# Kernel optimization log

Hardware: AMD Instinct MI355X
Metric: run time of the kernel (lower is better)

## Reference

```python
import jax, jax.numpy as jnp
import numpy as np

B, H, Q, K, D = 2, 8, 512, 512, 64


def setup_inputs() -> dict:
    key = jax.random.key(0)
    ks = jax.random.split(key, 8)
    s = 1.0 / np.sqrt(D)
    return {
        "query": jax.random.normal(ks[0], (B, H, Q, D), dtype=jnp.float32),
        "keys": jax.random.normal(ks[1], (B, H, K, D), dtype=jnp.float32),
        "Wa_w": jax.random.normal(ks[2], (D, D), dtype=jnp.float32) * s,
        "Wa_b": jax.random.normal(ks[3], (D,), dtype=jnp.float32) * s,
        "Ua_w": jax.random.normal(ks[4], (D, D), dtype=jnp.float32) * s,
        "Ua_b": jax.random.normal(ks[5], (D,), dtype=jnp.float32) * s,
        "V_w": jax.random.normal(ks[6], (D,), dtype=jnp.float32) * s,
        "V_b": jax.random.normal(ks[7], (1,), dtype=jnp.float32) * s,
    }


def reference(query, keys, Wa_w, Wa_b, Ua_w, Ua_b, V_w, V_b):
    # Linear projections (torch Linear: x @ W.T + b)
    q_proj = jnp.einsum("bhqd,ed->bhqe", query, Wa_w) + Wa_b  # [B,H,Q,D]
    k_proj = jnp.einsum("bhkd,ed->bhke", keys, Ua_w) + Ua_b   # [B,H,K,D]
    # Broadcast add + tanh -> [B,H,Q,K,D] (the fusion-headroom intermediate)
    features = jnp.tanh(q_proj[:, :, :, None, :] + k_proj[:, :, None, :, :])
    # Linear reduce D -> scalar, squeeze last dim
    scores = jnp.einsum("bhqkd,d->bhqk", features, V_w) + V_b[0]  # [B,H,Q,K]
    return scores
```

## Files before the change

kernel.cpp:

```cpp
#include <hip/hip_runtime.h>


#define BHX 16
#define SEQ 512
#define DDIM 64
#define QT 32
#define KT 64

typedef float f4 __attribute__((ext_vector_type(4)));

__global__ __launch_bounds__(256) void proj_kernel(
    const float* __restrict__ query, const float* __restrict__ keys,
    const float* __restrict__ Wa_w,  const float* __restrict__ Wa_b,
    const float* __restrict__ Ua_w,  const float* __restrict__ Ua_b,
    float* __restrict__ eq, float* __restrict__ gk)
{
  const int t = threadIdx.x, lane = t & 63, wave = t >> 6;
  const bool is_k = blockIdx.x >= 512;
  const float* __restrict__ X  = is_k ? keys : query;
  const float* __restrict__ W  = is_k ? Ua_w : Wa_w;
  const float* __restrict__ Bv = is_k ? Ua_b : Wa_b;
  float* __restrict__ out      = is_k ? gk : eq;
  const int row0 = (blockIdx.x & 511) * 16;

  float w[64];
  const float4* W4 = (const float4*)(W + lane * DDIM);
#pragma unroll
  for (int i = 0; i < 16; ++i) {
    float4 v = W4[i];
    w[4*i] = v.x; w[4*i+1] = v.y; w[4*i+2] = v.z; w[4*i+3] = v.w;
  }

  const float C = 2.885390081777926815f;
  const float b = Bv[lane];

#pragma unroll 1
  for (int i = 0; i < 4; ++i) {
    const int r   = row0 + wave * 4 + i;
    const int off = __builtin_amdgcn_readfirstlane(r * DDIM);
    const float* xr = X + off;
    float a0 = 0, a1 = 0, a2 = 0, a3 = 0;
#pragma unroll
    for (int e = 0; e < 64; e += 4) {
      a0 = __builtin_fmaf(xr[e],     w[e],     a0);
      a1 = __builtin_fmaf(xr[e + 1], w[e + 1], a1);
      a2 = __builtin_fmaf(xr[e + 2], w[e + 2], a2);
      a3 = __builtin_fmaf(xr[e + 3], w[e + 3], a3);
    }
    float p = ((a0 + a1) + (a2 + a3)) + b;
    out[(size_t)r * DDIM + lane] = __builtin_amdgcn_exp2f(C * p);
  }
}

__device__ __forceinline__ void tree8(const float* __restrict__ A,
                                      const float* __restrict__ vw,
                                      float& num, float& P)
{
  const float n01 = __builtin_fmaf(vw[1], A[0], vw[0] * A[1]);
  const float n23 = __builtin_fmaf(vw[3], A[2], vw[2] * A[3]);
  const float n45 = __builtin_fmaf(vw[5], A[4], vw[4] * A[5]);
  const float n67 = __builtin_fmaf(vw[7], A[6], vw[6] * A[7]);
  const float P01 = A[0] * A[1], P23 = A[2] * A[3];
  const float P45 = A[4] * A[5], P67 = A[6] * A[7];
  const float n0123 = __builtin_fmaf(n23, P01, n01 * P23);
  const float n4567 = __builtin_fmaf(n67, P45, n45 * P67);
  const float P0123 = P01 * P23, P4567 = P45 * P67;
  num = __builtin_fmaf(n4567, P0123, n0123 * P4567);
  P   = P0123 * P4567;
}

__global__ __launch_bounds__(256) void score_kernel(
    const float* __restrict__ eq,
    const float* __restrict__ gk,
    const float* __restrict__ Vw,
    const float* __restrict__ Vb,
    float* __restrict__ out)
{
  __shared__ float gk_l[DDIM][KT + 1];
  __shared__ float ql[QT * DDIM];

  const int bh   = blockIdx.z;
  const int q0   = blockIdx.y * QT;
  const int k0   = blockIdx.x * KT;
  const int t    = threadIdx.x;
  const int lane = t & 63;
  const int wave = t >> 6;

  {
    const float* base = gk + (size_t)(bh * SEQ + k0 + wave * 16) * DDIM;
#pragma unroll
    for (int i = 0; i < 16; ++i)
      gk_l[lane][wave * 16 + i] = base[i * DDIM + lane];
  }
  {
    const float4* src = (const float4*)(eq + (size_t)(bh * SEQ + q0) * DDIM);
    float4* dst = (float4*)ql;
    dst[t]       = src[t];
    dst[t + 256] = src[t + 256];
  }

  float acc0 = Vb[0];
#pragma unroll
  for (int d = 0; d < 64; ++d) acc0 += Vw[d];

  __syncthreads();

  float acc[8] = {0.f, 0.f, 0.f, 0.f, 0.f, 0.f, 0.f, 0.f};
  const int qrow0 = wave * 8;

#pragma unroll 1
  for (int g = 0; g < 4; ++g) {
    float G[16];
#pragma unroll
    for (int j = 0; j < 16; ++j) G[j] = gk_l[16 * g + j][lane];
    float vwl[16];
#pragma unroll
    for (int j = 0; j < 16; ++j) vwl[j] = Vw[16 * g + j];

#pragma unroll
    for (int qi = 0; qi < 8; ++qi) {
      const f4* ev = (const f4*)(ql + (qrow0 + qi) * DDIM + 16 * g);
      float A[16];
#pragma unroll
      for (int j = 0; j < 4; ++j) {
        const f4 e = ev[j];
        A[4*j]     = __builtin_fmaf(e.x, G[4*j],     1.0f);
        A[4*j + 1] = __builtin_fmaf(e.y, G[4*j + 1], 1.0f);
        A[4*j + 2] = __builtin_fmaf(e.z, G[4*j + 2], 1.0f);
        A[4*j + 3] = __builtin_fmaf(e.w, G[4*j + 3], 1.0f);
      }
      float numA, PA, numB, PB;
      tree8(A,     vwl,     numA, PA);
      tree8(A + 8, vwl + 8, numB, PB);
      const float num = __builtin_fmaf(numA, PB, numB * PA);
      acc[qi] = __builtin_fmaf(num, __builtin_amdgcn_rcpf(PA * PB), acc[qi]);
    }
  }

  const size_t obase = (size_t)(bh * SEQ + q0 + qrow0) * SEQ + k0 + lane;
#pragma unroll
  for (int qi = 0; qi < 8; ++qi)
    out[obase + (size_t)qi * SEQ] = __builtin_fmaf(-2.f, acc[qi], acc0);
}

extern "C" void kernel_launch(void* const* d_in, const int* in_sizes, int n_in,
                              void* d_out, int out_size, void* d_ws, size_t ws_size,
                              hipStream_t stream) {
  const float* query = (const float*)d_in[0];
  const float* keys  = (const float*)d_in[1];
  const float* Wa_w  = (const float*)d_in[2];
  const float* Wa_b  = (const float*)d_in[3];
  const float* Ua_w  = (const float*)d_in[4];
  const float* Ua_b  = (const float*)d_in[5];
  const float* V_w   = (const float*)d_in[6];
  const float* V_b   = (const float*)d_in[7];
  float* out = (float*)d_out;

  const int R = BHX * SEQ;
  float* eq = (float*)d_ws;
  float* gk = eq + (size_t)R * DDIM;

  proj_kernel<<<1024, 256, 0, stream>>>(query, keys, Wa_w, Wa_b,
                                        Ua_w, Ua_b, eq, gk);

  dim3 grid(SEQ / KT, SEQ / QT, BHX);
  score_kernel<<<grid, 256, 0, stream>>>(eq, gk, V_w, V_b, out);
}
```

Baseline: 47.72 us.

## Use packed FP32 FMA with interleaved LDS layout in score kernel

After: 42.17 us. 1.13x faster.

```diff
diff --git a/kernel.cpp b/kernel.cpp
--- a/kernel.cpp
+++ b/kernel.cpp
@@ -8,6 +8,11 @@
 #define KT 64
 
 typedef float f4 __attribute__((ext_vector_type(4)));
+typedef float f2 __attribute__((ext_vector_type(2)));
+
+__device__ __forceinline__ f2 pkfma(f2 a, f2 b, f2 c) {
+  return __builtin_elementwise_fma(a, b, c);
+}
 
 __global__ __launch_bounds__(256) void proj_kernel(
     const float* __restrict__ query, const float* __restrict__ keys,
@@ -16,12 +21,12 @@
     float* __restrict__ eq, float* __restrict__ gk)
 {
   const int t = threadIdx.x, lane = t & 63, wave = t >> 6;
-  const bool is_k = blockIdx.x >= 512;
+  const bool is_k = blockIdx.x >= 256;
   const float* __restrict__ X  = is_k ? keys : query;
   const float* __restrict__ W  = is_k ? Ua_w : Wa_w;
   const float* __restrict__ Bv = is_k ? Ua_b : Wa_b;
   float* __restrict__ out      = is_k ? gk : eq;
-  const int row0 = (blockIdx.x & 511) * 16;
+  const int row0 = (blockIdx.x & 255) * 32;
 
   float w[64];
   const float4* W4 = (const float4*)(W + lane * DDIM);
@@ -35,8 +40,8 @@
   const float b = Bv[lane];
 
 #pragma unroll 1
-  for (int i = 0; i < 4; ++i) {
-    const int r   = row0 + wave * 4 + i;
+  for (int i = 0; i < 8; ++i) {
+    const int r   = row0 + wave * 8 + i;
     const int off = __builtin_amdgcn_readfirstlane(r * DDIM);
     const float* xr = X + off;
     float a0 = 0, a1 = 0, a2 = 0, a3 = 0;
@@ -52,23 +57,6 @@
   }
 }
 
-__device__ __forceinline__ void tree8(const float* __restrict__ A,
-                                      const float* __restrict__ vw,
-                                      float& num, float& P)
-{
-  const float n01 = __builtin_fmaf(vw[1], A[0], vw[0] * A[1]);
-  const float n23 = __builtin_fmaf(vw[3], A[2], vw[2] * A[3]);
-  const float n45 = __builtin_fmaf(vw[5], A[4], vw[4] * A[5]);
-  const float n67 = __builtin_fmaf(vw[7], A[6], vw[6] * A[7]);
-  const float P01 = A[0] * A[1], P23 = A[2] * A[3];
-  const float P45 = A[4] * A[5], P67 = A[6] * A[7];
-  const float n0123 = __builtin_fmaf(n23, P01, n01 * P23);
-  const float n4567 = __builtin_fmaf(n67, P45, n45 * P67);
-  const float P0123 = P01 * P23, P4567 = P45 * P67;
-  num = __builtin_fmaf(n4567, P0123, n0123 * P4567);
-  P   = P0123 * P4567;
-}
-
 __global__ __launch_bounds__(256) void score_kernel(
     const float* __restrict__ eq,
     const float* __restrict__ gk,
@@ -76,7 +64,7 @@
     const float* __restrict__ Vb,
     float* __restrict__ out)
 {
-  __shared__ float gk_l[DDIM][KT + 1];
+  __shared__ float gkl[32][2 * KT + 2];
   __shared__ float ql[QT * DDIM];
 
   const int bh   = blockIdx.z;
@@ -88,15 +76,28 @@
 
   {
     const float* base = gk + (size_t)(bh * SEQ + k0 + wave * 16) * DDIM;
+    const int j  = lane & 31;
+    const int hi = lane >> 5;
 #pragma unroll
-    for (int i = 0; i < 16; ++i)
-      gk_l[lane][wave * 16 + i] = base[i * DDIM + lane];
+    for (int i = 0; i < 16; ++i) {
+      const int k = wave * 16 + i;
+      gkl[j][2 * k + hi] = base[i * DDIM + lane];
+    }
   }
   {
     const float4* src = (const float4*)(eq + (size_t)(bh * SEQ + q0) * DDIM);
-    float4* dst = (float4*)ql;
-    dst[t]       = src[t];
-    dst[t + 256] = src[t + 256];
+#pragma unroll
+    for (int half = 0; half < 2; ++half) {
+      const float4 v = src[t + 256 * half];
+      const int q  = (t >> 4) + 16 * half;
+      const int d0 = (t & 15) * 4;
+      float* row = ql + q * DDIM;
+      const int p0 = (d0 < 32) ? 2 * d0 : 2 * (d0 - 32) + 1;
+      row[p0]     = v.x;
+      row[p0 + 2] = v.y;
+      row[p0 + 4] = v.z;
+      row[p0 + 6] = v.w;
+    }
   }
 
   float acc0 = Vb[0];
@@ -105,42 +106,66 @@
 
   __syncthreads();
 
-  float acc[8] = {0.f, 0.f, 0.f, 0.f, 0.f, 0.f, 0.f, 0.f};
+  f2 acc2[8];
+#pragma unroll
+  for (int qi = 0; qi < 8; ++qi) acc2[qi] = f2{0.f, 0.f};
   const int qrow0 = wave * 8;
+  const f2 one2 = {1.0f, 1.0f};
 
 #pragma unroll 1
-  for (int g = 0; g < 4; ++g) {
-    float G[16];
+  for (int g = 0; g < 2; ++g) {
+    f2 Gp[16];
 #pragma unroll
-    for (int j = 0; j < 16; ++j) G[j] = gk_l[16 * g + j][lane];
-    float vwl[16];
+    for (int j = 0; j < 16; ++j)
+      Gp[j] = *(const f2*)&gkl[16 * g + j][2 * lane];
+    f2 vwp[16];
 #pragma unroll
-    for (int j = 0; j < 16; ++j) vwl[j] = Vw[16 * g + j];
+    for (int j = 0; j < 16; ++j)
+      vwp[j] = f2{Vw[16 * g + j], Vw[16 * g + j + 32]};
 
 #pragma unroll
     for (int qi = 0; qi < 8; ++qi) {
-      const f4* ev = (const f4*)(ql + (qrow0 + qi) * DDIM + 16 * g);
-      float A[16];
+      const f4* ev = (const f4*)(ql + (qrow0 + qi) * DDIM + 32 * g);
+      f2 A[16];
 #pragma unroll
-      for (int j = 0; j < 4; ++j) {
-        const f4 e = ev[j];
-        A[4*j]     = __builtin_fmaf(e.x, G[4*j],     1.0f);
-        A[4*j + 1] = __builtin_fmaf(e.y, G[4*j + 1], 1.0f);
-        A[4*j + 2] = __builtin_fmaf(e.z, G[4*j + 2], 1.0f);
-        A[4*j + 3] = __builtin_fmaf(e.w, G[4*j + 3], 1.0f);
+      for (int u = 0; u < 8; ++u) {
+        const f4 e = ev[u];
+        A[2*u]     = pkfma(f2{e.x, e.y}, Gp[2*u],     one2);
+        A[2*u + 1] = pkfma(f2{e.z, e.w}, Gp[2*u + 1], one2);
       }
-      float numA, PA, numB, PB;
-      tree8(A,     vwl,     numA, PA);
-      tree8(A + 8, vwl + 8, numB, PB);
-      const float num = __builtin_fmaf(numA, PB, numB * PA);
-      acc[qi] = __builtin_fmaf(num, __builtin_amdgcn_rcpf(PA * PB), acc[qi]);
+      f2 n1[8], P1[8];
+#pragma unroll
+      for (int u = 0; u < 8; ++u) {
+        n1[u] = pkfma(vwp[2*u + 1], A[2*u], vwp[2*u] * A[2*u + 1]);
+        P1[u] = A[2*u] * A[2*u + 1];
+      }
+      f2 n2[4], P2[4];
+#pragma unroll
+      for (int u = 0; u < 4; ++u) {
+        n2[u] = pkfma(n1[2*u + 1], P1[2*u], n1[2*u] * P1[2*u + 1]);
+        P2[u] = P1[2*u] * P1[2*u + 1];
+      }
+      f2 n3[2], P3[2];
+#pragma unroll
+      for (int u = 0; u < 2; ++u) {
+        n3[u] = pkfma(n2[2*u + 1], P2[2*u], n2[2*u] * P2[2*u + 1]);
+        P3[u] = P2[2*u] * P2[2*u + 1];
+      }
+      const f2 n4 = pkfma(n3[1], P3[0], n3[0] * P3[1]);
+      const f2 P4 = P3[0] * P3[1];
+      f2 r2;
+      r2.x = __builtin_amdgcn_rcpf(P4.x);
+      r2.y = __builtin_amdgcn_rcpf(P4.y);
+      acc2[qi] = pkfma(n4, r2, acc2[qi]);
     }
   }
 
   const size_t obase = (size_t)(bh * SEQ + q0 + qrow0) * SEQ + k0 + lane;
 #pragma unroll
-  for (int qi = 0; qi < 8; ++qi)
-    out[obase + (size_t)qi * SEQ] = __builtin_fmaf(-2.f, acc[qi], acc0);
+  for (int qi = 0; qi < 8; ++qi) {
+    const float a = acc2[qi].x + acc2[qi].y;
+    out[obase + (size_t)qi * SEQ] = __builtin_fmaf(-2.f, a, acc0);
+  }
 }
 
 extern "C" void kernel_launch(void* const* d_in, const int* in_sizes, int n_in,
@@ -160,8 +185,8 @@
   float* eq = (float*)d_ws;
   float* gk = eq + (size_t)R * DDIM;
 
-  proj_kernel<<<1024, 256, 0, stream>>>(query, keys, Wa_w, Wa_b,
-                                        Ua_w, Ua_b, eq, gk);
+  proj_kernel<<<512, 256, 0, stream>>>(query, keys, Wa_w, Wa_b,
+                                       Ua_w, Ua_b, eq, gk);
 
   dim3 grid(SEQ / KT, SEQ / QT, BHX);
   score_kernel<<<grid, 256, 0, stream>>>(eq, gk, V_w, V_b, out);
```

## Load key projections directly from global, shrink fraction groups, raise occupancy

Applied to the files above, without the earlier changes.

Measured after the change: 47.52 us. Within noise of the previous version (-0.4%).

```diff
diff --git a/kernel.cpp b/kernel.cpp
--- a/kernel.cpp
+++ b/kernel.cpp
@@ -16,12 +16,12 @@
     float* __restrict__ eq, float* __restrict__ gk)
 {
   const int t = threadIdx.x, lane = t & 63, wave = t >> 6;
-  const bool is_k = blockIdx.x >= 512;
+  const bool is_k = blockIdx.x >= 256;
   const float* __restrict__ X  = is_k ? keys : query;
   const float* __restrict__ W  = is_k ? Ua_w : Wa_w;
   const float* __restrict__ Bv = is_k ? Ua_b : Wa_b;
   float* __restrict__ out      = is_k ? gk : eq;
-  const int row0 = (blockIdx.x & 511) * 16;
+  const int row0 = (blockIdx.x & 255) * 32;
 
   float w[64];
   const float4* W4 = (const float4*)(W + lane * DDIM);
@@ -35,8 +35,8 @@
   const float b = Bv[lane];
 
 #pragma unroll 1
-  for (int i = 0; i < 4; ++i) {
-    const int r   = row0 + wave * 4 + i;
+  for (int i = 0; i < 8; ++i) {
+    const int r   = row0 + wave * 8 + i;
     const int off = __builtin_amdgcn_readfirstlane(r * DDIM);
     const float* xr = X + off;
     float a0 = 0, a1 = 0, a2 = 0, a3 = 0;
@@ -52,31 +52,13 @@
   }
 }
 
-__device__ __forceinline__ void tree8(const float* __restrict__ A,
-                                      const float* __restrict__ vw,
-                                      float& num, float& P)
-{
-  const float n01 = __builtin_fmaf(vw[1], A[0], vw[0] * A[1]);
-  const float n23 = __builtin_fmaf(vw[3], A[2], vw[2] * A[3]);
-  const float n45 = __builtin_fmaf(vw[5], A[4], vw[4] * A[5]);
-  const float n67 = __builtin_fmaf(vw[7], A[6], vw[6] * A[7]);
-  const float P01 = A[0] * A[1], P23 = A[2] * A[3];
-  const float P45 = A[4] * A[5], P67 = A[6] * A[7];
-  const float n0123 = __builtin_fmaf(n23, P01, n01 * P23);
-  const float n4567 = __builtin_fmaf(n67, P45, n45 * P67);
-  const float P0123 = P01 * P23, P4567 = P45 * P67;
-  num = __builtin_fmaf(n4567, P0123, n0123 * P4567);
-  P   = P0123 * P4567;
-}
-
-__global__ __launch_bounds__(256) void score_kernel(
+__global__ __launch_bounds__(256, 8) void score_kernel(
     const float* __restrict__ eq,
     const float* __restrict__ gk,
     const float* __restrict__ Vw,
     const float* __restrict__ Vb,
     float* __restrict__ out)
 {
-  __shared__ float gk_l[DDIM][KT + 1];
   __shared__ float ql[QT * DDIM];
 
   const int bh   = blockIdx.z;
@@ -86,12 +68,6 @@
   const int lane = t & 63;
   const int wave = t >> 6;
 
-  {
-    const float* base = gk + (size_t)(bh * SEQ + k0 + wave * 16) * DDIM;
-#pragma unroll
-    for (int i = 0; i < 16; ++i)
-      gk_l[lane][wave * 16 + i] = base[i * DDIM + lane];
-  }
   {
     const float4* src = (const float4*)(eq + (size_t)(bh * SEQ + q0) * DDIM);
     float4* dst = (float4*)ql;
@@ -107,33 +83,42 @@
 
   float acc[8] = {0.f, 0.f, 0.f, 0.f, 0.f, 0.f, 0.f, 0.f};
   const int qrow0 = wave * 8;
+  const float* gbase = gk + (size_t)(bh * SEQ + k0 + lane) * DDIM;
 
 #pragma unroll 1
-  for (int g = 0; g < 4; ++g) {
-    float G[16];
+  for (int g = 0; g < 8; ++g) {
+    const f4 G0 = *(const f4*)(gbase + 8 * g);
+    const f4 G1 = *(const f4*)(gbase + 8 * g + 4);
+    float vw[8];
 #pragma unroll
-    for (int j = 0; j < 16; ++j) G[j] = gk_l[16 * g + j][lane];
-    float vwl[16];
-#pragma unroll
-    for (int j = 0; j < 16; ++j) vwl[j] = Vw[16 * g + j];
+    for (int j = 0; j < 8; ++j) vw[j] = Vw[8 * g + j];
 
 #pragma unroll
     for (int qi = 0; qi < 8; ++qi) {
-      const f4* ev = (const f4*)(ql + (qrow0 + qi) * DDIM + 16 * g);
-      float A[16];
-#pragma unroll
-      for (int j = 0; j < 4; ++j) {
-        const f4 e = ev[j];
-        A[4*j]     = __builtin_fmaf(e.x, G[4*j],     1.0f);
-        A[4*j + 1] = __builtin_fmaf(e.y, G[4*j + 1], 1.0f);
-        A[4*j + 2] = __builtin_fmaf(e.z, G[4*j + 2], 1.0f);
-        A[4*j + 3] = __builtin_fmaf(e.w, G[4*j + 3], 1.0f);
-      }
-      float numA, PA, numB, PB;
-      tree8(A,     vwl,     numA, PA);
-      tree8(A + 8, vwl + 8, numB, PB);
-      const float num = __builtin_fmaf(numA, PB, numB * PA);
-      acc[qi] = __builtin_fmaf(num, __builtin_amdgcn_rcpf(PA * PB), acc[qi]);
+      const f4* ev = (const f4*)(ql + (qrow0 + qi) * DDIM + 8 * g);
+      const f4 e0 = ev[0];
+      const f4 e1 = ev[1];
+      float A[8];
+      A[0] = __builtin_fmaf(e0.x, G0.x, 1.0f);
+      A[1] = __builtin_fmaf(e0.y, G0.y, 1.0f);
+      A[2] = __builtin_fmaf(e0.z, G0.z, 1.0f);
+      A[3] = __builtin_fmaf(e0.w, G0.w, 1.0f);
+      A[4] = __builtin_fmaf(e1.x, G1.x, 1.0f);
+      A[5] = __builtin_fmaf(e1.y, G1.y, 1.0f);
+      A[6] = __builtin_fmaf(e1.z, G1.z, 1.0f);
+      A[7] = __builtin_fmaf(e1.w, G1.w, 1.0f);
+      const float n01 = __builtin_fmaf(vw[1], A[0], vw[0] * A[1]);
+      const float n23 = __builtin_fmaf(vw[3], A[2], vw[2] * A[3]);
+      const float n45 = __builtin_fmaf(vw[5], A[4], vw[4] * A[5]);
+      const float n67 = __builtin_fmaf(vw[7], A[6], vw[6] * A[7]);
+      const float P01 = A[0] * A[1], P23 = A[2] * A[3];
+      const float P45 = A[4] * A[5], P67 = A[6] * A[7];
+      const float n0123 = __builtin_fmaf(n23, P01, n01 * P23);
+      const float n4567 = __builtin_fmaf(n67, P45, n45 * P67);
+      const float P0123 = P01 * P23, P4567 = P45 * P67;
+      const float num = __builtin_fmaf(n4567, P0123, n0123 * P4567);
+      const float P   = P0123 * P4567;
+      acc[qi] = __builtin_fmaf(num, __builtin_amdgcn_rcpf(P), acc[qi]);
     }
   }
 
@@ -160,8 +145,8 @@
   float* eq = (float*)d_ws;
   float* gk = eq + (size_t)R * DDIM;
 
-  proj_kernel<<<1024, 256, 0, stream>>>(query, keys, Wa_w, Wa_b,
-                                        Ua_w, Ua_b, eq, gk);
+  proj_kernel<<<512, 256, 0, stream>>>(query, keys, Wa_w, Wa_b,
+                                       Ua_w, Ua_b, eq, gk);
 
   dim3 grid(SEQ / KT, SEQ / QT, BHX);
   score_kernel<<<grid, 256, 0, stream>>>(eq, gk, V_w, V_b, out);
```
